# Kernel optimization log

Hardware: AMD Instinct MI355X
Metric: run time of the kernel (lower is better)

## Reference

```python
import jax, jax.numpy as jnp
import numpy as np

B, P, D, H, K = 8, 1024, 768, 12, 16
GRID = 32
TEMP = 0.1
CANTOR_W = 0.3
NEG = -1e9


def _cantor_bias():
    # Cantor pairing fingerprints -> pairwise affinity bias (LearnedWormholeRouter init)
    pos = np.arange(P)
    xg = pos % GRID
    yg = pos // GRID
    s = xg + yg
    z = (s * (s + 1) // 2 + yg).astype(np.float32)
    fp = z / max(z.max(), 1.0)
    aff = 1.0 - np.abs(fp[None, :] - fp[:, None])
    np.fill_diagonal(aff, NEG)
    return jnp.asarray(aff * CANTOR_W, dtype=jnp.float32)


def setup_inputs() -> dict:
    key = jax.random.key(0)
    ks = jax.random.split(key, 4)
    sc = 1.0 / np.sqrt(D)
    x = jax.random.normal(ks[0], (B, P + 1, D), jnp.float32)
    Wq = jax.random.normal(ks[1], (D, D), jnp.float32) * sc
    Wk = jax.random.normal(ks[2], (D, D), jnp.float32) * sc
    Wv = jax.random.normal(ks[3], (D, D), jnp.float32) * sc
    zb = jnp.zeros((D,), jnp.float32)
    return {"x": x, "Wq": Wq, "bq": zb, "Wk": Wk, "bk": zb,
            "Wv": Wv, "bv": zb, "pos_bias": _cantor_bias()}


def _l2norm(t):
    # torch F.normalize(dim=-1, eps=1e-12)
    n = jnp.linalg.norm(t, axis=-1, keepdims=True)
    return t / jnp.maximum(n, 1e-12)


def reference(x, Wq, bq, Wk, bk, Wv, bv, pos_bias):
    Dh = D // H
    xp = x[:, 1:, :]                                   # [B,P,D] drop CLS
    q = _l2norm(xp @ Wq + bq)                          # [B,P,D]
    k = _l2norm(xp @ Wk + bk)
    scores = jnp.einsum('bpd,bqd->bpq', q, k) + pos_bias
    scores = jnp.where(jnp.eye(P, dtype=bool), NEG, scores)
    topk_scores, routes = jax.lax.top_k(scores / TEMP, K)   # [B,P,K]
    weights = jax.nn.softmax(topk_scores, axis=-1)          # [B,P,K]
    # per-head values
    v = (xp @ Wv + bv).reshape(x.shape[0], P, H, Dh).transpose(0, 2, 1, 3)  # [B,H,P,Dh]
    # gather_wormhole_multihead: routes shared across heads -> [B,H,P,K,Dh]
    gathered = jax.vmap(lambda vb, rb: vb[:, rb, :])(v, routes)
    out = jnp.einsum('bpk,bhpkd->bhpd', weights, gathered)  # weighted wormhole combine
    return out.transpose(0, 2, 1, 3).reshape(x.shape[0], P, D)
```

## Files before the change

### kernel.cpp

```cpp
#include <hip/hip_runtime.h>
#include <math.h>

#define B_   8
#define P_   1024
#define D_   768
#define NEGV -1000000000.0f

__global__ __launch_bounds__(256) void gemm_qkv_np(
    const float* __restrict__ x,
    const float* __restrict__ Wq, const float* __restrict__ bq,
    const float* __restrict__ Wk, const float* __restrict__ bk,
    const float* __restrict__ Wv, const float* __restrict__ bv,
    float* __restrict__ Qo, float* __restrict__ Ko, float* __restrict__ Vo)
{
    const int which = blockIdx.z;
    const float* __restrict__ W    = (which == 0) ? Wq : (which == 1) ? Wk : Wv;
    const float* __restrict__ bias = (which == 0) ? bq : (which == 1) ? bk : bv;
    float* __restrict__ Out        = (which == 0) ? Qo : (which == 1) ? Ko : Vo;

    const int n0 = blockIdx.x * 128;
    const int m0 = blockIdx.y * 128;
    const int t  = threadIdx.x;
    const int tx = t & 15, ty = t >> 4;

    __shared__ float As[16 * 132];
    __shared__ float Bs[16 * 132];

    const int  ra  = t >> 2, ca = t & 3;
    const int  ar0 = m0 + ra;
    const int  ar1 = m0 + ra + 64;
    const long a_off0 = ((long)(ar0 >> 10) * 1025 + 1 + (ar0 & 1023)) * D_;
    const long a_off1 = ((long)(ar1 >> 10) * 1025 + 1 + (ar1 & 1023)) * D_;
    const int  db = t >> 5, cb = t & 31;

    float acc[8][8]  = {};
    float acc1[8][8] = {};

    for (int d0 = 0; d0 < D_; d0 += 16) {
        float4 av0 = *reinterpret_cast<const float4*>(x + a_off0 + d0 + 4 * ca);
        float4 av1 = *reinterpret_cast<const float4*>(x + a_off1 + d0 + 4 * ca);
        float4 bw0 = *reinterpret_cast<const float4*>(W + (long)(d0 + db) * D_ + n0 + 4 * cb);
        float4 bw1 = *reinterpret_cast<const float4*>(W + (long)(d0 + db + 8) * D_ + n0 + 4 * cb);
        __syncthreads();
        As[(4 * ca + 0) * 132 + ra]      = av0.x;
        As[(4 * ca + 1) * 132 + ra]      = av0.y;
        As[(4 * ca + 2) * 132 + ra]      = av0.z;
        As[(4 * ca + 3) * 132 + ra]      = av0.w;
        As[(4 * ca + 0) * 132 + ra + 64] = av1.x;
        As[(4 * ca + 1) * 132 + ra + 64] = av1.y;
        As[(4 * ca + 2) * 132 + ra + 64] = av1.z;
        As[(4 * ca + 3) * 132 + ra + 64] = av1.w;
        *reinterpret_cast<float4*>(&Bs[db * 132 + 4 * cb])       = bw0;
        *reinterpret_cast<float4*>(&Bs[(db + 8) * 132 + 4 * cb]) = bw1;
        __syncthreads();
#pragma unroll
        for (int d = 0; d < 16; ++d) {
            float4 a0 = *reinterpret_cast<const float4*>(&As[d * 132 + 8 * ty]);
            float4 a1 = *reinterpret_cast<const float4*>(&As[d * 132 + 8 * ty + 4]);
            float4 b0 = *reinterpret_cast<const float4*>(&Bs[d * 132 + 8 * tx]);
            float4 b1 = *reinterpret_cast<const float4*>(&Bs[d * 132 + 8 * tx + 4]);
            float a[8] = {a0.x, a0.y, a0.z, a0.w, a1.x, a1.y, a1.z, a1.w};
            float b[8] = {b0.x, b0.y, b0.z, b0.w, b1.x, b1.y, b1.z, b1.w};
#pragma unroll
            for (int i = 0; i < 8; ++i)
#pragma unroll
                for (int j = 0; j < 8; ++j)
                    acc[i][j] = fmaf(a[i], b[j], acc[i][j]);
        }
        if (d0 == 368) {
#pragma unroll
            for (int i = 0; i < 8; ++i)
#pragma unroll
                for (int j = 0; j < 8; ++j) { acc1[i][j] = acc[i][j]; acc[i][j] = 0.0f; }
        }
    }

    float bcol[8];
#pragma unroll
    for (int u = 0; u < 2; ++u) {
        float4 bb = *reinterpret_cast<const float4*>(bias + n0 + 8 * tx + 4 * u);
        bcol[4 * u + 0] = bb.x; bcol[4 * u + 1] = bb.y;
        bcol[4 * u + 2] = bb.z; bcol[4 * u + 3] = bb.w;
    }
#pragma unroll
    for (int i = 0; i < 8; ++i) {
        const long r = m0 + 8 * ty + i;
        float* orow = Out + r * D_ + n0 + 8 * tx;
#pragma unroll
        for (int u = 0; u < 2; ++u) {
            float4 o;
            float s0 = __fadd_rn(acc1[i][4 * u + 0], acc[i][4 * u + 0]);
            float s1 = __fadd_rn(acc1[i][4 * u + 1], acc[i][4 * u + 1]);
            float s2 = __fadd_rn(acc1[i][4 * u + 2], acc[i][4 * u + 2]);
            float s3 = __fadd_rn(acc1[i][4 * u + 3], acc[i][4 * u + 3]);
            o.x = __fadd_rn(s0, bcol[4 * u + 0]);
            o.y = __fadd_rn(s1, bcol[4 * u + 1]);
            o.z = __fadd_rn(s2, bcol[4 * u + 2]);
            o.w = __fadd_rn(s3, bcol[4 * u + 3]);
            *reinterpret_cast<float4*>(orow + 4 * u) = o;
        }
    }
}

__global__ __launch_bounds__(256) void l2norm_np(float* __restrict__ Q,
                                                 float* __restrict__ K)
{
    const int gid  = blockIdx.x * 256 + threadIdx.x;
    const int w    = gid >> 6;
    const int lane = gid & 63;
    const int wl   = threadIdx.x >> 6;
    float* __restrict__ base = (w < 8192) ? Q : K;
    const long row = (long)(w & 8191);
    float* p = base + row * D_;

    const int bb = lane >> 3, jj = lane & 7;
    const float* seg = p + 96 * bb + jj;
    float r = 0.0f;
#pragma unroll
    for (int i = 0; i < 12; ++i) {
        float xv = seg[8 * i];
        r = __fadd_rn(r, __fmul_rn(xv, xv));
    }

    __shared__ float red[4][64];
    red[wl][lane] = r;
    __syncthreads();

    float Bv[8];
#pragma unroll
    for (int b2 = 0; b2 < 8; ++b2) {
        const float* rr = &red[wl][8 * b2];
        float t1 = __fadd_rn(rr[0], rr[1]);
        float t2 = __fadd_rn(rr[2], rr[3]);
        float t3 = __fadd_rn(rr[4], rr[5]);
        float t4 = __fadd_rn(rr[6], rr[7]);
        Bv[b2] = __fadd_rn(__fadd_rn(t1, t2), __fadd_rn(t3, t4));
    }
    float s01 = __fadd_rn(Bv[0], Bv[1]), s23 = __fadd_rn(Bv[2], Bv[3]);
    float s45 = __fadd_rn(Bv[4], Bv[5]), s67 = __fadd_rn(Bv[6], Bv[7]);
    float tot = __fadd_rn(__fadd_rn(s01, s23), __fadd_rn(s45, s67));

    const float nm = fmaxf(__fsqrt_rn(tot), 1e-12f);

    float* q = p + lane * 12;
#pragma unroll
    for (int i = 0; i < 12; ++i) q[i] = __fdiv_rn(q[i], nm);
}

__global__ __launch_bounds__(256) void scores_np(
    const float* __restrict__ Q, const float* __restrict__ K,
    const float* __restrict__ pb, float* __restrict__ S)
{
    const int bz = blockIdx.z;
    const int n0 = blockIdx.x * 32;
    const int m0 = blockIdx.y * 32;
    const int t  = threadIdx.x;
    const int q    = t & 3;
    const int quad = t >> 2;
    const int qx   = quad & 7;
    const int qy   = quad >> 3;

    __shared__ float Qs[16 * 36];
    __shared__ float Ks[16 * 36];

    const float* Qb = Q + (((long)bz << 10) + m0) * D_;
    const float* Kb = K + (((long)bz << 10) + n0) * D_;

    const int sr = (t & 127) >> 2;
    const int sg = t & 3;
    const float* gsrc = (t < 128) ? (Qb + (long)sr * D_ + 4 * sg)
                                  : (Kb + (long)sr * D_ + 4 * sg);
    float* lw = (t < 128) ? Qs : Ks;

    float acc[4][4][4] = {};

    for (int d0 = 0; d0 < D_; d0 += 16) {
        __syncthreads();
        float4 g = *reinterpret_cast<const float4*>(gsrc + d0);
        lw[(4 * sg + 0) * 36 + sr] = g.x;
        lw[(4 * sg + 1) * 36 + sr] = g.y;
        lw[(4 * sg + 2) * 36 + sr] = g.z;
        lw[(4 * sg + 3) * 36 + sr] = g.w;
        __syncthreads();

#pragma unroll
        for (int s = 0; s < 4; ++s) {
            const int dd = q + 4 * s;
            float4 qv = *reinterpret_cast<const float4*>(&Qs[dd * 36 + 4 * qy]);
            float4 kv = *reinterpret_cast<const float4*>(&Ks[dd * 36 + 4 * qx]);
            float a[4] = {qv.x, qv.y, qv.z, qv.w};
            float b[4] = {kv.x, kv.y, kv.z, kv.w};
#pragma unroll
            for (int i = 0; i < 4; ++i)
#pragma unroll
                for (int j = 0; j < 4; ++j)
                    acc[s][i][j] = fmaf(a[i], b[j], acc[s][i][j]);
        }
    }

    float dot[4][4];
#pragma unroll
    for (int i = 0; i < 4; ++i)
#pragma unroll
        for (int j = 0; j < 4; ++j) {
            float ylo = __fadd_rn(acc[0][i][j], acc[2][i][j]);
            float yhi = __fadd_rn(acc[1][i][j], acc[3][i][j]);
            float zz  = __fadd_rn(ylo, yhi);
            float zr  = __shfl_xor(zz, 2, 64);
            float t2  = __fadd_rn(zz, zr);
            float tr  = __shfl_xor(t2, 1, 64);
            dot[i][j] = __fadd_rn(t2, tr);
        }

    if (q == 0) {
        const int c0 = n0 + 4 * qx;
#pragma unroll
        for (int i = 0; i < 4; ++i) {
            const int p = m0 + 4 * qy + i;
            float4 pbv = *reinterpret_cast<const float4*>(pb + (long)p * P_ + c0);
            float v[4] = {__fadd_rn(dot[i][0], pbv.x), __fadd_rn(dot[i][1], pbv.y),
                          __fadd_rn(dot[i][2], pbv.z), __fadd_rn(dot[i][3], pbv.w)};
#pragma unroll
            for (int j = 0; j < 4; ++j)
                if (c0 + j == p) v[j] = NEGV;
            float4 o = {v[0], v[1], v[2], v[3]};
            *reinterpret_cast<float4*>(S + (((long)bz << 10) + p) * P_ + c0) = o;
        }
    }
}

__global__ __launch_bounds__(256) void topk_np(
    const float* __restrict__ S, const float* __restrict__ V,
    float* __restrict__ out)
{
    const int gid  = blockIdx.x * 256 + threadIdx.x;
    const int gw   = gid >> 6;
    const int lane = gid & 63;
    const int b    = gw >> 10;

    const float* srow = S + ((long)gw << 10);
    float s[16];
#pragma unroll
    for (int t = 0; t < 16; ++t) s[t] = __fdiv_rn(srow[lane + 64 * t], 0.1f);

    float topv[16];
    int   topi[16];
#pragma unroll
    for (int r = 0; r < 16; ++r) {
        float bvv = s[0];
        int   bt  = 0;
#pragma unroll
        for (int t = 1; t < 16; ++t)
            if (s[t] > bvv) { bvv = s[t]; bt = t; }
        int bi = lane + 64 * bt;
#pragma unroll
        for (int m = 1; m < 64; m <<= 1) {
            float ov = __shfl_xor(bvv, m, 64);
            int   oi = __shfl_xor(bi, m, 64);
            if (ov > bvv || (ov == bvv && oi < bi)) { bvv = ov; bi = oi; }
        }
        topv[r] = bvv;
        topi[r] = bi;
#pragma unroll
        for (int t = 0; t < 16; ++t)
            if (lane + 64 * t == bi) s[t] = -3.0e38f;
    }

    const float mx = topv[0];
    float e[16];
#pragma unroll
    for (int r = 0; r < 16; ++r) e[r] = expf(topv[r] - mx);
    float r8[8];
#pragma unroll
    for (int j = 0; j < 8; ++j) r8[j] = __fadd_rn(e[j], e[j + 8]);
    float t1 = __fadd_rn(r8[0], r8[1]);
    float t2 = __fadd_rn(r8[2], r8[3]);
    float t3 = __fadd_rn(r8[4], r8[5]);
    float t4 = __fadd_rn(r8[6], r8[7]);
    float sum = __fadd_rn(__fadd_rn(t1, t2), __fadd_rn(t3, t4));
    float wgt[16];
#pragma unroll
    for (int r = 0; r < 16; ++r) wgt[r] = __fdiv_rn(e[r], sum);

    float4 a0 = {0, 0, 0, 0}, a1 = {0, 0, 0, 0}, a2 = {0, 0, 0, 0};
    const float* vb = V + ((long)b << 10) * D_;
#pragma unroll
    for (int r = 0; r < 16; ++r) {
        const float* vr = vb + (long)topi[r] * D_ + lane * 12;
        const float wr = wgt[r];
        float4 x0 = *reinterpret_cast<const float4*>(vr);
        float4 x1 = *reinterpret_cast<const float4*>(vr + 4);
        float4 x2 = *reinterpret_cast<const float4*>(vr + 8);
        a0.x = fmaf(wr, x0.x, a0.x); a0.y = fmaf(wr, x0.y, a0.y);
        a0.z = fmaf(wr, x0.z, a0.z); a0.w = fmaf(wr, x0.w, a0.w);
        a1.x = fmaf(wr, x1.x, a1.x); a1.y = fmaf(wr, x1.y, a1.y);
        a1.z = fmaf(wr, x1.z, a1.z); a1.w = fmaf(wr, x1.w, a1.w);
        a2.x = fmaf(wr, x2.x, a2.x); a2.y = fmaf(wr, x2.y, a2.y);
        a2.z = fmaf(wr, x2.z, a2.z); a2.w = fmaf(wr, x2.w, a2.w);
    }
    float* orow = out + (long)gw * D_ + lane * 12;
    *reinterpret_cast<float4*>(orow)     = a0;
    *reinterpret_cast<float4*>(orow + 4) = a1;
    *reinterpret_cast<float4*>(orow + 8) = a2;
}

extern "C" void kernel_launch(void* const* d_in, const int* in_sizes, int n_in,
                              void* d_out, int out_size, void* d_ws, size_t ws_size,
                              hipStream_t stream)
{
    const float* x  = (const float*)d_in[0];
    const float* Wq = (const float*)d_in[1];
    const float* bq = (const float*)d_in[2];
    const float* Wk = (const float*)d_in[3];
    const float* bk = (const float*)d_in[4];
    const float* Wv = (const float*)d_in[5];
    const float* bv = (const float*)d_in[6];
    const float* pb = (const float*)d_in[7];
    float* out = (float*)d_out;

    float* ws = (float*)d_ws;
    float* Q = ws;
    float* K = Q + (size_t)B_ * P_ * D_;
    float* V = K + (size_t)B_ * P_ * D_;
    float* S = V + (size_t)B_ * P_ * D_;

    hipLaunchKernelGGL(gemm_qkv_np, dim3(6, 64, 3), dim3(256), 0, stream,
                       x, Wq, bq, Wk, bk, Wv, bv, Q, K, V);
    hipLaunchKernelGGL(l2norm_np, dim3(4096), dim3(256), 0, stream, Q, K);
    hipLaunchKernelGGL(scores_np, dim3(32, 32, 8), dim3(256), 0, stream,
                       Q, K, pb, S);
    hipLaunchKernelGGL(topk_np, dim3(2048), dim3(256), 0, stream,
                       S, V, out);
}
```

Measured before the change: 841.6 us.

## Double-buffer QKV GEMM shared tiles and spill first-half partial sums to output

The QKV projection GEMM now uses two shared-memory buffers so the global loads for the next K-slice overlap the FMA work on the current slice, which removes one barrier per iteration. The separate 64-register acc1 array that held the first half of the reduction is gone. That partial sum is written to the output buffer after the first pass and read back before the final add. This lowers register pressure and may raise occupancy, but it adds an extra global write and read per output tile and doubles shared memory use.

```diff
diff --git a/kernel.cpp b/kernel.cpp
--- a/kernel.cpp
+++ b/kernel.cpp
@@ -23,8 +23,8 @@
     const int t  = threadIdx.x;
     const int tx = t & 15, ty = t >> 4;
 
-    __shared__ float As[16 * 132];
-    __shared__ float Bs[16 * 132];
+    __shared__ float As[2][16 * 132];
+    __shared__ float Bs[2][16 * 132];
 
     const int  ra  = t >> 2, ca = t & 3;
     const int  ar0 = m0 + ra;
@@ -33,47 +33,85 @@
     const long a_off1 = ((long)(ar1 >> 10) * 1025 + 1 + (ar1 & 1023)) * D_;
     const int  db = t >> 5, cb = t & 31;
 
-    float acc[8][8]  = {};
-    float acc1[8][8] = {};
-
-    for (int d0 = 0; d0 < D_; d0 += 16) {
-        float4 av0 = *reinterpret_cast<const float4*>(x + a_off0 + d0 + 4 * ca);
-        float4 av1 = *reinterpret_cast<const float4*>(x + a_off1 + d0 + 4 * ca);
-        float4 bw0 = *reinterpret_cast<const float4*>(W + (long)(d0 + db) * D_ + n0 + 4 * cb);
-        float4 bw1 = *reinterpret_cast<const float4*>(W + (long)(d0 + db + 8) * D_ + n0 + 4 * cb);
+    const float* xa0 = x + a_off0 + 4 * ca;
+    const float* xa1 = x + a_off1 + 4 * ca;
+    const float* wb0 = W + (long)db * D_ + n0 + 4 * cb;
+    const float* wb1 = W + (long)(db + 8) * D_ + n0 + 4 * cb;
+
+    float acc[8][8] = {};
+
+    auto stage = [&](int bsel, const float4& av0, const float4& av1,
+                     const float4& bw0, const float4& bw1) {
+        float* A  = As[bsel];
+        float* Bx = Bs[bsel];
+        A[(4 * ca + 0) * 132 + ra]      = av0.x;
+        A[(4 * ca + 1) * 132 + ra]      = av0.y;
+        A[(4 * ca + 2) * 132 + ra]      = av0.z;
+        A[(4 * ca + 3) * 132 + ra]      = av0.w;
+        A[(4 * ca + 0) * 132 + ra + 64] = av1.x;
+        A[(4 * ca + 1) * 132 + ra + 64] = av1.y;
+        A[(4 * ca + 2) * 132 + ra + 64] = av1.z;
+        A[(4 * ca + 3) * 132 + ra + 64] = av1.w;
+        *reinterpret_cast<float4*>(&Bx[db * 132 + 4 * cb])       = bw0;
+        *reinterpret_cast<float4*>(&Bx[(db + 8) * 132 + 4 * cb]) = bw1;
+    };
+
+    auto run_pass = [&](int dstart) {
+        float4 av0 = *reinterpret_cast<const float4*>(xa0 + dstart);
+        float4 av1 = *reinterpret_cast<const float4*>(xa1 + dstart);
+        float4 bw0 = *reinterpret_cast<const float4*>(wb0 + (long)dstart * D_);
+        float4 bw1 = *reinterpret_cast<const float4*>(wb1 + (long)dstart * D_);
         __syncthreads();
-        As[(4 * ca + 0) * 132 + ra]      = av0.x;
-        As[(4 * ca + 1) * 132 + ra]      = av0.y;
-        As[(4 * ca + 2) * 132 + ra]      = av0.z;
-        As[(4 * ca + 3) * 132 + ra]      = av0.w;
-        As[(4 * ca + 0) * 132 + ra + 64] = av1.x;
-        As[(4 * ca + 1) * 132 + ra + 64] = av1.y;
-        As[(4 * ca + 2) * 132 + ra + 64] = av1.z;
-        As[(4 * ca + 3) * 132 + ra + 64] = av1.w;
-        *reinterpret_cast<float4*>(&Bs[db * 132 + 4 * cb])       = bw0;
-        *reinterpret_cast<float4*>(&Bs[(db + 8) * 132 + 4 * cb]) = bw1;
+        stage(0, av0, av1, bw0, bw1);
         __syncthreads();
-#pragma unroll
-        for (int d = 0; d < 16; ++d) {
-            float4 a0 = *reinterpret_cast<const float4*>(&As[d * 132 + 8 * ty]);
-            float4 a1 = *reinterpret_cast<const float4*>(&As[d * 132 + 8 * ty + 4]);
-            float4 b0 = *reinterpret_cast<const float4*>(&Bs[d * 132 + 8 * tx]);
-            float4 b1 = *reinterpret_cast<const float4*>(&Bs[d * 132 + 8 * tx + 4]);
-            float a[8] = {a0.x, a0.y, a0.z, a0.w, a1.x, a1.y, a1.z, a1.w};
-            float b[8] = {b0.x, b0.y, b0.z, b0.w, b1.x, b1.y, b1.z, b1.w};
-#pragma unroll
-            for (int i = 0; i < 8; ++i)
-#pragma unroll
-                for (int j = 0; j < 8; ++j)
-                    acc[i][j] = fmaf(a[i], b[j], acc[i][j]);
-        }
-        if (d0 == 368) {
-#pragma unroll
-            for (int i = 0; i < 8; ++i)
-#pragma unroll
-                for (int j = 0; j < 8; ++j) { acc1[i][j] = acc[i][j]; acc[i][j] = 0.0f; }
-        }
-    }
+
+        for (int it = 0; it < 24; ++it) {
+            const int cur = it & 1;
+            if (it < 23) {
+                const int dn = dstart + 16 * (it + 1);
+                av0 = *reinterpret_cast<const float4*>(xa0 + dn);
+                av1 = *reinterpret_cast<const float4*>(xa1 + dn);
+                bw0 = *reinterpret_cast<const float4*>(wb0 + (long)dn * D_);
+                bw1 = *reinterpret_cast<const float4*>(wb1 + (long)dn * D_);
+            }
+            const float* Ab = As[cur];
+            const float* Bb = Bs[cur];
+#pragma unroll
+            for (int d = 0; d < 16; ++d) {
+                float4 a0 = *reinterpret_cast<const float4*>(&Ab[d * 132 + 8 * ty]);
+                float4 a1 = *reinterpret_cast<const float4*>(&Ab[d * 132 + 8 * ty + 4]);
+                float4 b0 = *reinterpret_cast<const float4*>(&Bb[d * 132 + 8 * tx]);
+                float4 b1 = *reinterpret_cast<const float4*>(&Bb[d * 132 + 8 * tx + 4]);
+                float a[8] = {a0.x, a0.y, a0.z, a0.w, a1.x, a1.y, a1.z, a1.w};
+                float b[8] = {b0.x, b0.y, b0.z, b0.w, b1.x, b1.y, b1.z, b1.w};
+#pragma unroll
+                for (int i = 0; i < 8; ++i)
+#pragma unroll
+                    for (int j = 0; j < 8; ++j)
+                        acc[i][j] = fmaf(a[i], b[j], acc[i][j]);
+            }
+            if (it < 23) {
+                stage(1 - cur, av0, av1, bw0, bw1);
+                __syncthreads();
+            }
+        }
+    };
+
+    run_pass(0);
+
+#pragma unroll
+    for (int i = 0; i < 8; ++i) {
+        const long r = m0 + 8 * ty + i;
+        float* orow = Out + r * D_ + n0 + 8 * tx;
+        float4 o0 = {acc[i][0], acc[i][1], acc[i][2], acc[i][3]};
+        float4 o1 = {acc[i][4], acc[i][5], acc[i][6], acc[i][7]};
+        *reinterpret_cast<float4*>(orow)     = o0;
+        *reinterpret_cast<float4*>(orow + 4) = o1;
+#pragma unroll
+        for (int j = 0; j < 8; ++j) acc[i][j] = 0.0f;
+    }
+
+    run_pass(384);
 
     float bcol[8];
 #pragma unroll
@@ -86,13 +124,16 @@
     for (int i = 0; i < 8; ++i) {
         const long r = m0 + 8 * ty + i;
         float* orow = Out + r * D_ + n0 + 8 * tx;
+        float4 p10 = *reinterpret_cast<float4*>(orow);
+        float4 p11 = *reinterpret_cast<float4*>(orow + 4);
+        float p1[8] = {p10.x, p10.y, p10.z, p10.w, p11.x, p11.y, p11.z, p11.w};
 #pragma unroll
         for (int u = 0; u < 2; ++u) {
             float4 o;
-            float s0 = __fadd_rn(acc1[i][4 * u + 0], acc[i][4 * u + 0]);
-            float s1 = __fadd_rn(acc1[i][4 * u + 1], acc[i][4 * u + 1]);
-            float s2 = __fadd_rn(acc1[i][4 * u + 2], acc[i][4 * u + 2]);
-            float s3 = __fadd_rn(acc1[i][4 * u + 3], acc[i][4 * u + 3]);
+            float s0 = __fadd_rn(p1[4 * u + 0], acc[i][4 * u + 0]);
+            float s1 = __fadd_rn(p1[4 * u + 1], acc[i][4 * u + 1]);
+            float s2 = __fadd_rn(p1[4 * u + 2], acc[i][4 * u + 2]);
+            float s3 = __fadd_rn(p1[4 * u + 3], acc[i][4 * u + 3]);
             o.x = __fadd_rn(s0, bcol[4 * u + 0]);
             o.y = __fadd_rn(s1, bcol[4 * u + 1]);
             o.z = __fadd_rn(s2, bcol[4 * u + 2]);
```

New measurement: 932.8 us. +10.8%, slower.
